# Kernel optimization log

Hardware: AMD Instinct MI355X
Metric: run time of the kernel (lower is better)

## Reference

```python
import jax, jax.numpy as jnp
import numpy as np

B, T, C = 4, 2048, 1024
H = 16
HD = C // H


def setup_inputs() -> dict:
    key = jax.random.key(0)
    k1, k2, k3 = jax.random.split(key, 3)
    x = jax.random.normal(k1, (B, T, C), dtype=jnp.float32)
    w_qkv = jax.random.normal(k2, (C, 3 * C), dtype=jnp.float32) * (C ** -0.5)
    w_proj = jax.random.normal(k3, (C, C), dtype=jnp.float32) * (C ** -0.5)
    b_proj = jnp.zeros((C,), dtype=jnp.float32)
    return {"x": x, "w_qkv": w_qkv, "w_proj": w_proj, "b_proj": b_proj}


def reference(x, w_qkv, w_proj, b_proj):
    Bd, Td, Cd = x.shape
    scale = HD ** -0.5
    qkv = x @ w_qkv  # [B,T,3C]
    q, k, v = jnp.split(qkv, 3, axis=-1)
    # [B,H,T,HD]
    q = q.reshape(Bd, Td, H, HD).transpose(0, 2, 1, 3)
    k = k.reshape(Bd, Td, H, HD).transpose(0, 2, 1, 3)
    v = v.reshape(Bd, Td, H, HD).transpose(0, 2, 1, 3)
    att = jnp.einsum('bhqd,bhkd->bhqk', q, k) * scale
    causal = jnp.triu(jnp.ones((Td, Td), dtype=bool), k=1)
    att = jnp.where(causal, -jnp.inf, att)
    att = jax.nn.softmax(att, axis=-1)
    y = jnp.einsum('bhqk,bhkd->bhqd', att, v)
    y = y.transpose(0, 2, 1, 3).reshape(Bd, Td, Cd)
    return y @ w_proj + b_proj
```

## Files before the change

kernel.cpp:

```cpp
#include <hip/hip_runtime.h>

typedef unsigned short u16;
typedef __attribute__((ext_vector_type(8))) short short8;
typedef __attribute__((ext_vector_type(4))) short short4v;
typedef __attribute__((ext_vector_type(4))) float floatx4;
typedef __attribute__((ext_vector_type(4))) unsigned short ushort4v;

#define B_ 4
#define T_ 2048
#define C_ 1024
#define H_ 16
#define HD_ 64

template <bool V> struct BC { static constexpr bool value = V; };
template <int N> struct ICN { static constexpr int v = N; };

static __device__ __forceinline__ u16 f2bf(float f) {
  union { float f; unsigned int i; } c; c.f = f;
  unsigned int u = c.i;
  return (u16)((u + 0x7FFFu + ((u >> 16) & 1u)) >> 16);
}
static __device__ __forceinline__ unsigned pk2(float lo, float hi) {
  union { float f; unsigned u; } a, b; a.f = hi; b.f = lo;
  return __builtin_amdgcn_perm(a.u, b.u, 0x07060302u);
}
static __device__ __forceinline__ unsigned pk2r(float lo, float hi) {
  return (unsigned)f2bf(lo) | ((unsigned)f2bf(hi) << 16);
}

static __device__ __forceinline__ void gload16(const u16* g, u16* l) {
  __builtin_amdgcn_global_load_lds(
      (const __attribute__((address_space(1))) unsigned int*)(g),
      (__attribute__((address_space(3))) unsigned int*)(l), 16, 0, 0);
}

template <int N> static __device__ __forceinline__ void wait_vm_bar() {
  if constexpr (N == 6)
    asm volatile("s_waitcnt vmcnt(6)\n\ts_barrier" ::: "memory");
  else if constexpr (N == 4)
    asm volatile("s_waitcnt vmcnt(4)\n\ts_barrier" ::: "memory");
  else if constexpr (N == 0)
    asm volatile("s_waitcnt vmcnt(0)\n\ts_barrier" ::: "memory");
}

__global__ __launch_bounds__(256) void prep_k(const float* __restrict__ x,
                                              const float* __restrict__ w_qkv,
                                              const float* __restrict__ w_proj,
                                              u16* __restrict__ xbf,
                                              u16* __restrict__ wqkvT,
                                              u16* __restrict__ wprojT) {
  const int bid = blockIdx.x;
  if (bid < 8192) {
    const int i = bid * 256 + threadIdx.x;
    const float4 f = ((const float4*)x)[i];
    ushort4v o;
    o.x = f2bf(f.x); o.y = f2bf(f.y); o.z = f2bf(f.z); o.w = f2bf(f.w);
    *(ushort4v*)(xbf + (size_t)i * 4) = o;
    return;
  }
  __shared__ u16 tile[32][33];
  const float* in;
  u16* out;
  int R, Cc, tb;
  if (bid < 11264) {
    in = w_qkv; out = wqkvT; R = C_; Cc = 3 * C_; tb = bid - 8192;
  } else {
    in = w_proj; out = wprojT; R = C_; Cc = C_; tb = bid - 11264;
  }
  const int tpr = Cc / 32;
  const int bx = (tb % tpr) * 32;
  const int by = (tb / tpr) * 32;
  const int tx = threadIdx.x & 31;
  const int ty = threadIdx.x >> 5;
  #pragma unroll
  for (int i = ty; i < 32; i += 8)
    tile[i][tx] = f2bf(in[(size_t)(by + i) * Cc + bx + tx]);
  __syncthreads();
  #pragma unroll
  for (int i = ty; i < 32; i += 8)
    out[(size_t)(bx + i) * R + by + tx] = tile[tx][i];
}

template <int MODE, int NFR>
__global__ __launch_bounds__(256, 2) void gemm4w(const u16* __restrict__ A,
                                                 const u16* __restrict__ Bt,
                                                 u16* __restrict__ outb,
                                                 u16* __restrict__ outv,
                                                 float* __restrict__ outf,
                                                 const float* __restrict__ bias,
                                                 int M, int N) {
  constexpr int TN = NFR * 32;
  constexpr int BUFA = 4096;
  constexpr int BUFB = TN * 32;
  constexpr int BUF = BUFA + BUFB;
  constexpr int LPW = (8 + TN / 16) / 4;
  __shared__ __align__(16) u16 lds[3 * BUF];

  const int bid = blockIdx.x;
  const int xcd = bid & 7;
  const int loc = bid >> 3;
  const int tM = (xcd * 8 + (loc & 7)) * 128;
  const int tN = (loc >> 3) * TN;
  const int tid = threadIdx.x;
  const int wave = tid >> 6;
  const int lane = tid & 63;
  const int lr = lane & 15;
  const int quad = lane >> 4;
  const int wm = wave >> 1;
  const int wn = wave & 1;
  const int csw = (lr >> 1) & 3;
  const int srow = lane >> 2;
  const int skofs = ((lane & 3) ^ ((lane >> 3) & 3)) * 8;

  const u16* gbase[LPW];
  int ldst[LPW];
  #pragma unroll
  for (int j = 0; j < LPW; j++) {
    const int s = wave * LPW + j;
    if (s < 8) {
      gbase[j] = A + (size_t)(tM + s * 16 + srow) * 1024 + skofs;
      ldst[j] = s * 512;
    } else {
      gbase[j] = Bt + (size_t)(tN + (s - 8) * 16 + srow) * 1024 + skofs;
      ldst[j] = BUFA + (s - 8) * 512;
    }
  }

  const floatx4 zf = {0.f, 0.f, 0.f, 0.f};
  floatx4 acc[4][NFR];
  #pragma unroll
  for (int i = 0; i < 4; i++)
    #pragma unroll
    for (int j = 0; j < NFR; j++) acc[i][j] = zf;

  auto stage = [&](int t, int buf) {
    #pragma unroll
    for (int j = 0; j < LPW; j++)
      gload16(gbase[j] + t * 32, &lds[buf * BUF + ldst[j]]);
  };

  auto ktile = [&](int t, int buf, auto VM) {
    constexpr int vm = decltype(VM)::v;
    const u16* lA = &lds[buf * BUF];
    const u16* lB = lA + BUFA;
    short8 af[4], bfr[NFR];
    #pragma unroll
    for (int mt = 0; mt < 4; mt++)
      af[mt] = *(const short8*)(&lA[(wm * 64 + mt * 16 + lr) * 32 + ((quad ^ csw) * 8)]);
    #pragma unroll
    for (int nt = 0; nt < NFR; nt++)
      bfr[nt] = *(const short8*)(&lB[(wn * (NFR * 16) + nt * 16 + lr) * 32 + ((quad ^ csw) * 8)]);
    if constexpr (vm > 0) stage(t + 2, (buf + 2) % 3);
    __builtin_amdgcn_s_setprio(1);
    #pragma unroll
    for (int mt = 0; mt < 4; mt++)
      #pragma unroll
      for (int nt = 0; nt < NFR; nt++)
        acc[mt][nt] = __builtin_amdgcn_mfma_f32_16x16x32_bf16(af[mt], bfr[nt],
                                                              acc[mt][nt], 0, 0, 0);
    __builtin_amdgcn_s_setprio(0);
    if constexpr (vm > 0) wait_vm_bar<LPW>();
    else if constexpr (vm == 0) wait_vm_bar<0>();
  };

  stage(0, 0); stage(1, 1);
  wait_vm_bar<LPW>();

  for (int tb = 0; tb < 10; ++tb) {
    const int t = tb * 3;
    ktile(t,     0, ICN<LPW>{});
    ktile(t + 1, 1, ICN<LPW>{});
    ktile(t + 2, 2, ICN<LPW>{});
  }
  ktile(30, 0, ICN<0>{});
  ktile(31, 1, ICN<-1>{});

  if constexpr (MODE == 1) {
    if (tN >= 2 * C_) {
      asm volatile("s_barrier" ::: "memory");
      #pragma unroll
      for (int mt = 0; mt < 4; mt++) {
        const int pb = wm * 64 + (mt >> 1) * 32 + quad * 8 + (mt & 1) * 4;
        #pragma unroll
        for (int nt = 0; nt < NFR; nt++) {
          const int vrow = wn * (NFR * 16) + nt * 16 + lr;
          u16* p = &lds[vrow * 128 + (((pb >> 3) ^ (vrow & 7)) * 8) + (pb & 7)];
          *(uint2*)(p) = make_uint2(pk2r(acc[mt][nt][0], acc[mt][nt][1]),
                                    pk2r(acc[mt][nt][2], acc[mt][nt][3]));
        }
      }
      asm volatile("s_waitcnt lgkmcnt(0)\n\ts_barrier" ::: "memory");
      const int b = tM >> 11;
      const int t0b = tM & (T_ - 1);
      const int h0 = (tN - 2 * C_) >> 6;
      u16* vb = outv + (size_t)(b * H_ + h0) * HD_ * T_;
      #pragma unroll
      for (int i = 0; i < 16; i++) {
        const int lin = tid + i * 256;
        const int row = lin >> 4;
        const int cp = lin & 15;
        const short8 v = *(const short8*)(&lds[row * 128 + ((cp ^ (row & 7)) * 8)]);
        *(short8*)(vb + (size_t)row * T_ + t0b + cp * 8) = v;
      }
      return;
    }
    const float qs = (tN < C_) ? 0.18033688f : 1.0f;
    #pragma unroll
    for (int mt = 0; mt < 4; mt++) {
      const int m0 = tM + wm * 64 + mt * 16 + quad * 4;
      #pragma unroll
      for (int nt = 0; nt < NFR; nt++) {
        const int n = tN + wn * (NFR * 16) + nt * 16 + lr;
        #pragma unroll
        for (int r = 0; r < 4; r++)
          outb[(size_t)(m0 + r) * N + n] = f2bf(acc[mt][nt][r] * qs);
      }
    }
  } else {
    #pragma unroll
    for (int mt = 0; mt < 4; mt++) {
      const int m0 = tM + wm * 64 + mt * 16 + quad * 4;
      #pragma unroll
      for (int nt = 0; nt < NFR; nt++) {
        const int n = tN + wn * (NFR * 16) + nt * 16 + lr;
        const float bv = bias[n];
        #pragma unroll
        for (int r = 0; r < 4; r++)
          __builtin_nontemporal_store(acc[mt][nt][r] + bv,
                                      &outf[(size_t)(m0 + r) * N + n]);
      }
    }
  }
}

__global__ __launch_bounds__(256, 4) void attn_k(const u16* __restrict__ qkv,
                                                 const u16* __restrict__ vt,
                                                 u16* __restrict__ y) {
  __shared__ __align__(16) u16 Ks[2 * 4096];
  __shared__ __align__(16) u16 Vs[2 * 4096];
  const int bid = blockIdx.x;
  const int s = bid >> 3;
  const int qp = s >> 3;
  const int bh = ((s & 7) << 3) | (bid & 7);
  const int b = bh >> 4, h = bh & 15;
  const int tid = threadIdx.x;
  const int wave = tid >> 6;
  const int lane = tid & 63;
  const int lr = lane & 15;
  const int quad = lane >> 4;
  const int qtA = qp, qtB = 31 - qp;

  const int srow = lane >> 3;
  const int skofs = ((lane & 7) ^ ((lane >> 3) & 7)) * 8;
  const int gsw = lr & 7;

  const size_t RS = 3 * C_;
  const u16* qcol = qkv + (size_t)b * T_ * RS + h * HD_;
  const u16* kcol = qcol + C_;

  const size_t qrA = (size_t)(qtA * 64 + wave * 16 + lr) * RS;
  const size_t qrB = (size_t)(qtB * 64 + wave * 16 + lr) * RS;
  const short8 aq0A = *(const short8*)(qcol + qrA + quad * 8);
  const short8 aq1A = *(const short8*)(qcol + qrA + 32 + quad * 8);
  const short8 aq0B = *(const short8*)(qcol + qrB + quad * 8);
  const short8 aq1B = *(const short8*)(qcol + qrB + 32 + quad * 8);

  const floatx4 zf = {0.f, 0.f, 0.f, 0.f};
  const short8 vones = {16256, 16256, 16256, 16256, 16256, 16256, 16256, 16256};

  floatx4 accA[4], accB[4];
  floatx4 accSA = zf, accSB = zf;
  #pragma unroll
  for (int i = 0; i < 4; i++) { accA[i] = zf; accB[i] = zf; }

  auto stage = [&](int kt, int buf) {
    #pragma unroll
    for (int j = 0; j < 2; j++) {
      const int seg = wave * 2 + j;
      const int row = seg * 8 + srow;
      gload16(kcol + (size_t)(kt * 64 + row) * RS + skofs, &Ks[buf * 4096 + seg * 512]);
      gload16(vt + ((size_t)bh * HD_ + row) * T_ + kt * 64 + skofs, &Vs[buf * 4096 + seg * 512]);
    }
    __builtin_amdgcn_sched_barrier(0);
  };

  auto core = [&](int cur, auto WA, auto DA, auto DB) {
    constexpr bool wA = decltype(WA)::value;
    constexpr bool dA = decltype(DA)::value;
    constexpr bool dB = decltype(DB)::value;
    const u16* Kb = &Ks[cur * 4096];
    const u16* Vb = &Vs[cur * 4096];
    float peA[4][4], peB[4][4];
    #pragma unroll
    for (int nt = 0; nt < 4; nt++) {
      const short8 bk0 =
          *(const short8*)(&Kb[(nt * 16 + lr) * 64 + ((quad ^ gsw) * 8)]);
      const short8 bk1 =
          *(const short8*)(&Kb[(nt * 16 + lr) * 64 + (((quad + 4) ^ gsw) * 8)]);
      {
        floatx4 st = __builtin_amdgcn_mfma_f32_16x16x32_bf16(
            bk1, aq1B,
            __builtin_amdgcn_mfma_f32_16x16x32_bf16(bk0, aq0B, zf, 0, 0, 0),
            0, 0, 0);
        #pragma unroll
        for (int r = 0; r < 4; r++) {
          float pe = __builtin_amdgcn_exp2f(st[r]);
          if constexpr (dB)
            if (nt * 16 + quad * 4 + r > wave * 16 + lr) pe = 0.f;
          peB[nt][r] = pe;
        }
      }
      if constexpr (wA) {
        floatx4 st = __builtin_amdgcn_mfma_f32_16x16x32_bf16(
            bk1, aq1A,
            __builtin_amdgcn_mfma_f32_16x16x32_bf16(bk0, aq0A, zf, 0, 0, 0),
            0, 0, 0);
        #pragma unroll
        for (int r = 0; r < 4; r++) {
          float pe = __builtin_amdgcn_exp2f(st[r]);
          if constexpr (dA)
            if (nt * 16 + quad * 4 + r > wave * 16 + lr) pe = 0.f;
          peA[nt][r] = pe;
        }
      }
    }

    short8 pB[2], pA[2];
    #pragma unroll
    for (int h2 = 0; h2 < 2; h2++) {
      union { unsigned u[4]; short8 s8; } w;
      w.u[0] = pk2(peB[2 * h2][0], peB[2 * h2][1]);
      w.u[1] = pk2(peB[2 * h2][2], peB[2 * h2][3]);
      w.u[2] = pk2(peB[2 * h2 + 1][0], peB[2 * h2 + 1][1]);
      w.u[3] = pk2(peB[2 * h2 + 1][2], peB[2 * h2 + 1][3]);
      pB[h2] = w.s8;
    }
    if constexpr (wA) {
      #pragma unroll
      for (int h2 = 0; h2 < 2; h2++) {
        union { unsigned u[4]; short8 s8; } w;
        w.u[0] = pk2(peA[2 * h2][0], peA[2 * h2][1]);
        w.u[1] = pk2(peA[2 * h2][2], peA[2 * h2][3]);
        w.u[2] = pk2(peA[2 * h2 + 1][0], peA[2 * h2 + 1][1]);
        w.u[3] = pk2(peA[2 * h2 + 1][2], peA[2 * h2 + 1][3]);
        pA[h2] = w.s8;
      }
    }

    #pragma unroll
    for (int h2 = 0; h2 < 2; h2++) {
      accSB = __builtin_amdgcn_mfma_f32_16x16x32_bf16(vones, pB[h2], accSB, 0, 0, 0);
      if constexpr (wA)
        accSA = __builtin_amdgcn_mfma_f32_16x16x32_bf16(vones, pA[h2], accSA, 0, 0, 0);
      #pragma unroll
      for (int dt = 0; dt < 4; dt++) {
        const short8 av = *(const short8*)(
            &Vb[(dt * 16 + lr) * 64 + (((h2 * 4 + quad) ^ gsw) * 8)]);
        accB[dt] = __builtin_amdgcn_mfma_f32_16x16x32_bf16(av, pB[h2], accB[dt], 0, 0, 0);
        if constexpr (wA)
          accA[dt] = __builtin_amdgcn_mfma_f32_16x16x32_bf16(av, pA[h2], accA[dt], 0, 0, 0);
      }
    }
  };

  stage(0, 0);
  asm volatile("s_waitcnt vmcnt(0)\n\ts_barrier" ::: "memory");
  int cur = 0;
  for (int kt = 0; kt < qtA; kt++) {
    stage(kt + 1, cur ^ 1);
    core(cur, BC<true>{}, BC<false>{}, BC<false>{});
    asm volatile("s_waitcnt vmcnt(0)\n\ts_barrier" ::: "memory");
    cur ^= 1;
  }
  stage(qtA + 1, cur ^ 1);
  core(cur, BC<true>{}, BC<true>{}, BC<false>{});
  asm volatile("s_waitcnt vmcnt(0)\n\ts_barrier" ::: "memory");
  cur ^= 1;
  for (int kt = qtA + 1; kt < qtB; kt++) {
    stage(kt + 1, cur ^ 1);
    core(cur, BC<false>{}, BC<false>{}, BC<false>{});
    asm volatile("s_waitcnt vmcnt(0)\n\ts_barrier" ::: "memory");
    cur ^= 1;
  }
  core(cur, BC<false>{}, BC<false>{}, BC<true>{});

  #pragma unroll
  for (int ph = 0; ph < 2; ph++) {
    const int qt = ph ? qtB : qtA;
    const floatx4* acc = ph ? accB : accA;
    const float inv = 1.f / (ph ? accSB[0] : accSA[0]);
    const int qg = qt * 64 + wave * 16 + lr;
    u16* yrow = y + ((size_t)(b * T_ + qg)) * C_ + h * HD_;
    #pragma unroll
    for (int dt = 0; dt < 4; dt++) {
      ushort4v o;
      #pragma unroll
      for (int r = 0; r < 4; r++) o[r] = f2bf(acc[dt][r] * inv);
      *(ushort4v*)(yrow + dt * 16 + quad * 4) = o;
    }
  }
}

extern "C" void kernel_launch(void* const* d_in, const int* in_sizes, int n_in,
                              void* d_out, int out_size, void* d_ws, size_t ws_size,
                              hipStream_t stream) {
  const float* x      = (const float*)d_in[0];
  const float* w_qkv  = (const float*)d_in[1];
  const float* w_proj = (const float*)d_in[2];
  const float* b_proj = (const float*)d_in[3];
  float* out = (float*)d_out;

  u16* ws = (u16*)d_ws;
  const size_t SZ = (size_t)B_ * T_ * C_;
  u16* xbf    = ws;
  u16* wqkvT  = xbf + SZ;
  u16* wprojT = wqkvT + (size_t)3 * C_ * C_;
  u16* qkvw   = wprojT + (size_t)C_ * C_;
  u16* vtw    = qkvw + 3 * SZ;
  u16* yw     = xbf;

  prep_k<<<12288, 256, 0, stream>>>(x, w_qkv, w_proj, xbf, wqkvT, wprojT);
  gemm4w<1, 8><<<768, 256, 0, stream>>>(
      xbf, wqkvT, qkvw, vtw, nullptr, nullptr, B_ * T_, 3 * C_);
  attn_k<<<1024, 256, 0, stream>>>(qkvw, vtw, yw);
  gemm4w<2, 4><<<512, 256, 0, stream>>>(
      yw, wprojT, nullptr, nullptr, out, b_proj, B_ * T_, C_);
}
```

Measured before the change: 221.9 us.

## Replace QKV GEMM with 256x256-tile 8-wave kernel using 4-stage LDS pipeline

Adds a dedicated QKV projection GEMM that uses 256x256 output tiles, 512 threads and a four-slot LDS ring buffer. Each slice splits the MFMA work into two halves with barriers in between, and grid blocks are mapped to XCDs so each XCD covers a band of M rows. The existing gemm4w is reduced to the output-projection path only. The goal is more operand reuse per loaded byte and better L2 locality, at the cost of higher register and LDS use per block and fewer blocks (384), which may cause wave-quantization imbalance across CUs.

```diff
diff --git a/kernel.cpp b/kernel.cpp
--- a/kernel.cpp
+++ b/kernel.cpp
@@ -35,7 +35,9 @@
 }
 
 template <int N> static __device__ __forceinline__ void wait_vm_bar() {
-  if constexpr (N == 6)
+  if constexpr (N == 8)
+    asm volatile("s_waitcnt vmcnt(8)\n\ts_barrier" ::: "memory");
+  else if constexpr (N == 6)
     asm volatile("s_waitcnt vmcnt(6)\n\ts_barrier" ::: "memory");
   else if constexpr (N == 4)
     asm volatile("s_waitcnt vmcnt(4)\n\ts_barrier" ::: "memory");
@@ -79,6 +81,155 @@
   #pragma unroll
   for (int i = ty; i < 32; i += 8)
     out[(size_t)(bx + i) * R + by + tx] = tile[tx][i];
+}
+
+__global__ __launch_bounds__(512, 2)
+void gemm256(const u16* __restrict__ A, const u16* __restrict__ Bt,
+             u16* __restrict__ outb, u16* __restrict__ outv) {
+  constexpr int SLICE = 16384;
+  __shared__ __align__(16) u16 lds[4 * SLICE];
+
+  const int bid = blockIdx.x;
+  const int xcd = bid & 7;
+  const int loc = bid >> 3;
+  const int tM = (xcd * 4 + (loc & 3)) * 256;
+  const int tN = (loc >> 2) * 256;
+  const int tid = threadIdx.x;
+  const int wave = tid >> 6;
+  const int lane = tid & 63;
+  const int lr = lane & 15;
+  const int quad = lane >> 4;
+  const int wm = wave >> 2;
+  const int wn = wave & 3;
+  const int csw = (lr >> 1) & 3;
+  const int srow = lane >> 2;
+  const int skofs = ((lane & 3) ^ ((lane >> 3) & 3)) * 8;
+
+  const u16* gbase[4];
+  int ldst[4];
+  #pragma unroll
+  for (int j = 0; j < 4; j++) {
+    const int s = wave * 4 + j;
+    if (s < 16) {
+      gbase[j] = A + (size_t)(tM + s * 16 + srow) * 1024 + skofs;
+      ldst[j] = s * 512;
+    } else {
+      gbase[j] = Bt + (size_t)(tN + (s - 16) * 16 + srow) * 1024 + skofs;
+      ldst[j] = 8192 + (s - 16) * 512;
+    }
+  }
+
+  const floatx4 zf = {0.f, 0.f, 0.f, 0.f};
+  floatx4 acc[8][4];
+  #pragma unroll
+  for (int i = 0; i < 8; i++)
+    #pragma unroll
+    for (int j = 0; j < 4; j++) acc[i][j] = zf;
+
+  auto stage = [&](int t) {
+    #pragma unroll
+    for (int j = 0; j < 4; j++)
+      gload16(gbase[j] + t * 32, &lds[(t & 3) * SLICE + ldst[j]]);
+  };
+
+  short8 af[4], ag[4], bf[4];
+  auto readA = [&](int t, int mh, short8 (&f)[4]) {
+    const u16* p = &lds[(t & 3) * SLICE];
+    #pragma unroll
+    for (int mt = 0; mt < 4; mt++)
+      f[mt] = *(const short8*)(
+          &p[(wm * 128 + mh * 64 + mt * 16 + lr) * 32 + ((quad ^ csw) * 8)]);
+  };
+  auto readB = [&](int t) {
+    const u16* p = &lds[(t & 3) * SLICE + 8192];
+    #pragma unroll
+    for (int nt = 0; nt < 4; nt++)
+      bf[nt] = *(const short8*)(
+          &p[(wn * 64 + nt * 16 + lr) * 32 + ((quad ^ csw) * 8)]);
+  };
+  auto mfma16 = [&](int mh, short8 (&f)[4]) {
+    __builtin_amdgcn_s_setprio(1);
+    #pragma unroll
+    for (int mt = 0; mt < 4; mt++)
+      #pragma unroll
+      for (int nt = 0; nt < 4; nt++)
+        acc[mh * 4 + mt][nt] = __builtin_amdgcn_mfma_f32_16x16x32_bf16(
+            f[mt], bf[nt], acc[mh * 4 + mt][nt], 0, 0, 0);
+    __builtin_amdgcn_s_setprio(0);
+  };
+
+  auto slice = [&](int t, auto STG, auto VM) {
+    readA(t, 0, af);
+    readB(t);
+    if constexpr (decltype(STG)::value) stage(t + 3);
+    asm volatile("s_barrier" ::: "memory");
+    asm volatile("s_waitcnt lgkmcnt(0)" ::: "memory");
+    __builtin_amdgcn_sched_barrier(0);
+    mfma16(0, af);
+    asm volatile("s_barrier" ::: "memory");
+    readA(t, 1, ag);
+    asm volatile("s_barrier" ::: "memory");
+    asm volatile("s_waitcnt lgkmcnt(0)" ::: "memory");
+    __builtin_amdgcn_sched_barrier(0);
+    mfma16(1, ag);
+    constexpr int vm = decltype(VM)::v;
+    if constexpr (vm >= 0) wait_vm_bar<vm>();
+  };
+
+  stage(0); stage(1); stage(2);
+  wait_vm_bar<8>();
+
+  #pragma unroll 1
+  for (int t = 0; t < 29; t++) slice(t, BC<true>{}, ICN<8>{});
+  slice(29, BC<false>{}, ICN<4>{});
+  slice(30, BC<false>{}, ICN<0>{});
+  slice(31, BC<false>{}, ICN<-1>{});
+
+  if (tN >= 2 * C_) {
+    asm volatile("s_barrier" ::: "memory");
+    #pragma unroll
+    for (int mh = 0; mh < 2; mh++)
+      #pragma unroll
+      for (int mt = 0; mt < 4; mt++) {
+        const int pb = wm * 128 + mh * 64 + (mt >> 1) * 32 + quad * 8 + (mt & 1) * 4;
+        #pragma unroll
+        for (int nt = 0; nt < 4; nt++) {
+          const int vrow = wn * 64 + nt * 16 + lr;
+          u16* p = &lds[vrow * 256 + (((pb >> 3) ^ (vrow & 7)) * 8) + (pb & 7)];
+          *(uint2*)(p) =
+              make_uint2(pk2r(acc[mh * 4 + mt][nt][0], acc[mh * 4 + mt][nt][1]),
+                         pk2r(acc[mh * 4 + mt][nt][2], acc[mh * 4 + mt][nt][3]));
+        }
+      }
+    asm volatile("s_waitcnt lgkmcnt(0)\n\ts_barrier" ::: "memory");
+    const int b = tM >> 11;
+    const int t0b = tM & (T_ - 1);
+    const int h0 = (tN - 2 * C_) >> 6;
+    u16* vb = outv + (size_t)(b * H_ + h0) * HD_ * T_;
+    #pragma unroll
+    for (int i = 0; i < 16; i++) {
+      const int lin = tid + i * 512;
+      const int row = lin >> 5;
+      const int cp = lin & 31;
+      const short8 v = *(const short8*)(&lds[row * 256 + ((cp ^ (row & 7)) * 8)]);
+      *(short8*)(vb + (size_t)row * T_ + t0b + cp * 8) = v;
+    }
+    return;
+  }
+  const float qs = (tN < C_) ? 0.18033688f : 1.0f;
+  #pragma unroll
+  for (int mh = 0; mh < 2; mh++)
+    #pragma unroll
+    for (int mt = 0; mt < 4; mt++) {
+      const int m0 = tM + wm * 128 + mh * 64 + mt * 16 + quad * 4;
+      #pragma unroll
+      for (int nt = 0; nt < 4; nt++) {
+        const int n = tN + wn * 64 + nt * 16 + lr;
+        #pragma unroll
+        for (int r = 0; r < 4; r++)
+          outb[(size_t)(m0 + r) * (3 * C_) + n] = f2bf(acc[mh * 4 + mt][nt][r] * qs);
+      }
+    }
 }
 
 template <int MODE, int NFR>
@@ -175,60 +326,17 @@
   ktile(30, 0, ICN<0>{});
   ktile(31, 1, ICN<-1>{});
 
-  if constexpr (MODE == 1) {
-    if (tN >= 2 * C_) {
-      asm volatile("s_barrier" ::: "memory");
-      #pragma unroll
-      for (int mt = 0; mt < 4; mt++) {
-        const int pb = wm * 64 + (mt >> 1) * 32 + quad * 8 + (mt & 1) * 4;
-        #pragma unroll
-        for (int nt = 0; nt < NFR; nt++) {
-          const int vrow = wn * (NFR * 16) + nt * 16 + lr;
-          u16* p = &lds[vrow * 128 + (((pb >> 3) ^ (vrow & 7)) * 8) + (pb & 7)];
-          *(uint2*)(p) = make_uint2(pk2r(acc[mt][nt][0], acc[mt][nt][1]),
-                                    pk2r(acc[mt][nt][2], acc[mt][nt][3]));
-        }
-      }
-      asm volatile("s_waitcnt lgkmcnt(0)\n\ts_barrier" ::: "memory");
-      const int b = tM >> 11;
-      const int t0b = tM & (T_ - 1);
-      const int h0 = (tN - 2 * C_) >> 6;
-      u16* vb = outv + (size_t)(b * H_ + h0) * HD_ * T_;
-      #pragma unroll
-      for (int i = 0; i < 16; i++) {
-        const int lin = tid + i * 256;
-        const int row = lin >> 4;
-        const int cp = lin & 15;
-        const short8 v = *(const short8*)(&lds[row * 128 + ((cp ^ (row & 7)) * 8)]);
-        *(short8*)(vb + (size_t)row * T_ + t0b + cp * 8) = v;
-      }
-      return;
-    }
-    const float qs = (tN < C_) ? 0.18033688f : 1.0f;
-    #pragma unroll
-    for (int mt = 0; mt < 4; mt++) {
-      const int m0 = tM + wm * 64 + mt * 16 + quad * 4;
-      #pragma unroll
-      for (int nt = 0; nt < NFR; nt++) {
-        const int n = tN + wn * (NFR * 16) + nt * 16 + lr;
-        #pragma unroll
-        for (int r = 0; r < 4; r++)
-          outb[(size_t)(m0 + r) * N + n] = f2bf(acc[mt][nt][r] * qs);
-      }
-    }
-  } else {
-    #pragma unroll
-    for (int mt = 0; mt < 4; mt++) {
-      const int m0 = tM + wm * 64 + mt * 16 + quad * 4;
-      #pragma unroll
-      for (int nt = 0; nt < NFR; nt++) {
-        const int n = tN + wn * (NFR * 16) + nt * 16 + lr;
-        const float bv = bias[n];
-        #pragma unroll
-        for (int r = 0; r < 4; r++)
-          __builtin_nontemporal_store(acc[mt][nt][r] + bv,
-                                      &outf[(size_t)(m0 + r) * N + n]);
-      }
+  #pragma unroll
+  for (int mt = 0; mt < 4; mt++) {
+    const int m0 = tM + wm * 64 + mt * 16 + quad * 4;
+    #pragma unroll
+    for (int nt = 0; nt < NFR; nt++) {
+      const int n = tN + wn * (NFR * 16) + nt * 16 + lr;
+      const float bv = bias[n];
+      #pragma unroll
+      for (int r = 0; r < 4; r++)
+        __builtin_nontemporal_store(acc[mt][nt][r] + bv,
+                                    &outf[(size_t)(m0 + r) * N + n]);
     }
   }
 }
@@ -420,8 +528,7 @@
   u16* yw     = xbf;
 
   prep_k<<<12288, 256, 0, stream>>>(x, w_qkv, w_proj, xbf, wqkvT, wprojT);
-  gemm4w<1, 8><<<768, 256, 0, stream>>>(
-      xbf, wqkvT, qkvw, vtw, nullptr, nullptr, B_ * T_, 3 * C_);
+  gemm256<<<384, 512, 0, stream>>>(xbf, wqkvT, qkvw, vtw);
   attn_k<<<1024, 256, 0, stream>>>(qkvw, vtw, yw);
   gemm4w<2, 4><<<512, 256, 0, stream>>>(
       yw, wprojT, nullptr, nullptr, out, b_proj, B_ * T_, C_);
```

Result: slower. 236.5 us (+6.6%).
